# Optimization experiments

Hardware: AMD Instinct MI355X
Metric: run time of the kernel (lower is better)

The kernel has to match this reference:

```python
import jax, jax.numpy as jnp
import numpy as np

B, P, K = 32, 1024, 16  # clouds, points per cloud, neighbors


def setup_inputs() -> dict:
    key = jax.random.key(0)
    ks = jax.random.split(key, 5)
    N, C, H, D = B * P, 64, 128, 3
    x = jax.random.normal(ks[0], (N, C), dtype=jnp.float32)
    pos = jax.random.normal(ks[1], (N, D), dtype=jnp.float32)
    batch = jnp.arange(N, dtype=jnp.int64) // P  # cloud id per node
    W_e = jax.random.normal(ks[2], (2 * C, H), dtype=jnp.float32) * 0.05
    b_e = jnp.zeros((H,), dtype=jnp.float32)
    W_sc = jax.random.normal(ks[3], (C, H), dtype=jnp.float32) * 0.05
    b_sc = jnp.zeros((H,), dtype=jnp.float32)
    return {"x": x, "pos": pos, "batch": batch,
            "W_e": W_e, "b_e": b_e, "W_sc": W_sc, "b_sc": b_sc}


def _knn_idx(posb):
    # posb: [B, P, D] -> idx [B, P, K]: K nearest neighbors (sources) per target node,
    # within each cloud, excluding self (loop=False in torch_geometric.knn_graph).
    sq = jnp.sum(posb * posb, axis=-1)                       # [B, P]
    d2 = sq[:, :, None] + sq[:, None, :] - 2.0 * jnp.einsum('bid,bjd->bij', posb, posb)
    d2 = d2 + jnp.eye(P, dtype=posb.dtype)[None] * jnp.finfo(posb.dtype).max / 2
    _, idx = jax.lax.top_k(-d2, K)                           # [B, P, K]
    return idx


def reference(x, pos, batch, W_e, b_e, W_sc, b_sc):
    C = x.shape[-1]
    xb = x.reshape(B, P, C)
    posb = pos.reshape(B, P, -1)
    idx = _knn_idx(posb)                                     # [B, P, K]
    # gather neighbor (source) features per target node
    x_j = jax.vmap(lambda xc, ic: xc[ic])(xb, idx)           # [B, P, K, C]
    x_i = xb[:, :, None, :]                                  # [B, P, 1, C]
    # EdgeConv message: nn([x_i, x_j - x_i]), here Linear + ReLU
    e = jnp.concatenate([jnp.broadcast_to(x_i, x_j.shape), x_j - x_i], axis=-1)  # [B,P,K,2C]
    msg = jax.nn.relu(jnp.einsum('bpke,eh->bpkh', e, W_e) + b_e)
    agg = jnp.max(msg, axis=2)                               # max aggregation -> [B, P, H]
    shortcut = x @ W_sc + b_sc                               # [N, H]
    out = agg.reshape(-1, agg.shape[-1]) + shortcut
    return out
```

## Files before the change

### kernel.cpp

```cpp
#include <hip/hip_runtime.h>
#include <float.h>
#include <stdint.h>

#define BATCHES 32
#define P 1024
#define KNN 16
#define C 64
#define H 128
#define N (BATCHES * P)
#define NCOLS 384
#define SPLITS 8
#define CPS 128

typedef short short8 __attribute__((ext_vector_type(8)));
typedef float floatx4 __attribute__((ext_vector_type(4)));

__device__ __forceinline__ unsigned short f2bf(float f) {
    unsigned u = __float_as_uint(f);
    unsigned r = (u + 0x7FFF + ((u >> 16) & 1)) >> 16;
    return (unsigned short)r;
}

__global__ __launch_bounds__(256) void prep_w(
    const float* __restrict__ W_e, const float* __restrict__ b_e,
    const float* __restrict__ W_sc, const float* __restrict__ b_sc,
    unsigned short* __restrict__ WT, float* __restrict__ bias)
{
    int i = blockIdx.x * 256 + threadIdx.x;
    int col = i >> 6, c = i & 63;
    float w;
    if (col < 128)      w = W_e[c * 128 + col] - W_e[(64 + c) * 128 + col];
    else if (col < 256) w = W_e[(64 + c) * 128 + (col - 128)];
    else                w = W_sc[c * 128 + (col - 256)];
    WT[col * 64 + c] = f2bf(w);
    if (c == 0) {
        bias[col] = (col < 128) ? b_e[col] : (col < 256 ? 0.0f : b_sc[col - 256]);
    }
}

__global__ __launch_bounds__(512) void knn_kernel(
    const float* __restrict__ pos, int* __restrict__ idx_out)
{
    int t = threadIdx.x;
    int q = t & 63, s = t >> 6;
    int batch = blockIdx.x >> 4;
    int qblk  = blockIdx.x & 15;
    int iloc  = qblk * 64 + q;

    __shared__ float4 spos[P];
    __shared__ float  lists[SPLITS][16][64];
    __shared__ unsigned short elist[SPLITS][16][64];
    __shared__ int    ecnt[SPLITS][64];
    __shared__ float  Tq[64];

    const float* pb = pos + (size_t)batch * P * 3;
    for (int j = t; j < P; j += 512) {
        float x = pb[j * 3 + 0], y = pb[j * 3 + 1], z = pb[j * 3 + 2];
        float sq = __fadd_rn(__fadd_rn(__fmul_rn(x, x), __fmul_rn(y, y)),
                             __fmul_rn(z, z));
        spos[j] = make_float4(x, y, z, sq);
    }
    __syncthreads();

    float4 me = spos[iloc];
    float d[16];
#pragma unroll
    for (int k = 0; k < 16; ++k) d[k] = FLT_MAX;

    const int j0 = s * CPS;
    for (int jj = 0; jj < CPS; ++jj) {
        int j = j0 + jj;
        float4 c = spos[j];
        float dot = __fadd_rn(__fadd_rn(__fmul_rn(me.x, c.x), __fmul_rn(me.y, c.y)),
                              __fmul_rn(me.z, c.z));
        float d2 = __fadd_rn(__fadd_rn(me.w, c.w), __fmul_rn(-2.0f, dot));
        if (j == iloc) d2 = FLT_MAX;
#pragma unroll
        for (int k = 15; k >= 1; --k)
            d[k] = __builtin_amdgcn_fmed3f(d[k - 1], d2, d[k]);
        d[0] = fminf(d[0], d2);
    }
#pragma unroll
    for (int k = 0; k < 16; ++k) lists[s][k][q] = d[k];
    __syncthreads();

    if (s == 0) {
        float v0 = lists[0][0][q], v1 = lists[1][0][q];
        float v2 = lists[2][0][q], v3 = lists[3][0][q];
        float v4 = lists[4][0][q], v5 = lists[5][0][q];
        float v6 = lists[6][0][q], v7 = lists[7][0][q];
        int p0 = 0, p1 = 0, p2 = 0, p3 = 0, p4 = 0, p5 = 0, p6 = 0, p7 = 0;
        float T = 0.0f;
        for (int k = 0; k < 16; ++k) {
            float mn = fminf(fminf(fminf(v0, v1), fminf(v2, v3)),
                             fminf(fminf(v4, v5), fminf(v6, v7)));
            if      (v0 == mn) { p0++; v0 = (p0 < 16) ? lists[0][p0][q] : FLT_MAX; }
            else if (v1 == mn) { p1++; v1 = (p1 < 16) ? lists[1][p1][q] : FLT_MAX; }
            else if (v2 == mn) { p2++; v2 = (p2 < 16) ? lists[2][p2][q] : FLT_MAX; }
            else if (v3 == mn) { p3++; v3 = (p3 < 16) ? lists[3][p3][q] : FLT_MAX; }
            else if (v4 == mn) { p4++; v4 = (p4 < 16) ? lists[4][p4][q] : FLT_MAX; }
            else if (v5 == mn) { p5++; v5 = (p5 < 16) ? lists[5][p5][q] : FLT_MAX; }
            else if (v6 == mn) { p6++; v6 = (p6 < 16) ? lists[6][p6][q] : FLT_MAX; }
            else               { p7++; v7 = (p7 < 16) ? lists[7][p7][q] : FLT_MAX; }
            T = mn;
        }
        Tq[q] = T;
    }
    __syncthreads();
    float T = Tq[q];

    int cnt = 0;
    for (int jj = 0; jj < CPS; ++jj) {
        int j = j0 + jj;
        float4 c = spos[j];
        float dot = __fadd_rn(__fadd_rn(__fmul_rn(me.x, c.x), __fmul_rn(me.y, c.y)),
                              __fmul_rn(me.z, c.z));
        float d2 = __fadd_rn(__fadd_rn(me.w, c.w), __fmul_rn(-2.0f, dot));
        if (j == iloc) d2 = FLT_MAX;
        if (d2 <= T && cnt < 16) {
            elist[s][cnt][q] = (unsigned short)j;
            cnt++;
        }
    }
    ecnt[s][q] = cnt;
    __syncthreads();

    if (s == 0) {
        int out = 0;
        int gbase = (batch * P + iloc) * KNN;
        int base  = batch * P;
        for (int ss = 0; ss < SPLITS; ++ss) {
            int cc = ecnt[ss][q];
            for (int k = 0; k < cc && out < KNN; ++k) {
                idx_out[gbase + out] = base + (int)elist[ss][k][q];
                out++;
            }
        }
    }
}

__global__ __launch_bounds__(256) void gemm_kernel(
    const float* __restrict__ X, const unsigned short* __restrict__ WT,
    const float* __restrict__ bias,
    unsigned short* __restrict__ U, unsigned short* __restrict__ V,
    unsigned short* __restrict__ S)
{
    int t = threadIdx.x;
    int wave = t >> 6, l = t & 63;
    int m0 = (blockIdx.x * 4 + wave) * 16;
    int lm = l & 15, kg = l >> 4;

    const float4* arow = (const float4*)(X + (size_t)(m0 + lm) * 64 + kg * 8);
    float4 f0 = arow[0], f1 = arow[1];
    float4 f2 = arow[8], f3 = arow[9];
    short8 a0, a1;
    a0[0] = (short)f2bf(f0.x); a0[1] = (short)f2bf(f0.y);
    a0[2] = (short)f2bf(f0.z); a0[3] = (short)f2bf(f0.w);
    a0[4] = (short)f2bf(f1.x); a0[5] = (short)f2bf(f1.y);
    a0[6] = (short)f2bf(f1.z); a0[7] = (short)f2bf(f1.w);
    a1[0] = (short)f2bf(f2.x); a1[1] = (short)f2bf(f2.y);
    a1[2] = (short)f2bf(f2.z); a1[3] = (short)f2bf(f2.w);
    a1[4] = (short)f2bf(f3.x); a1[5] = (short)f2bf(f3.y);
    a1[6] = (short)f2bf(f3.z); a1[7] = (short)f2bf(f3.w);

#pragma unroll 4
    for (int nt = 0; nt < 24; ++nt) {
        const short8* brow = (const short8*)(WT + (size_t)(nt * 16 + lm) * 64 + kg * 8);
        short8 b0 = brow[0];
        short8 b1 = brow[4];
        floatx4 acc = {0.0f, 0.0f, 0.0f, 0.0f};
        acc = __builtin_amdgcn_mfma_f32_16x16x32_bf16(a0, b0, acc, 0, 0, 0);
        acc = __builtin_amdgcn_mfma_f32_16x16x32_bf16(a1, b1, acc, 0, 0, 0);

        int col = nt * 16 + lm;
        float bv = bias[col];
        unsigned short* dst; int cl;
        if (col < 128)      { dst = U; cl = col; }
        else if (col < 256) { dst = V; cl = col - 128; }
        else                { dst = S; cl = col - 256; }
#pragma unroll
        for (int r = 0; r < 4; ++r) {
            int row = m0 + kg * 4 + r;
            dst[(size_t)row * H + cl] = f2bf(acc[r] + bv);
        }
    }
}

__global__ __launch_bounds__(256) void final_kernel(
    const int* __restrict__ idx, const unsigned short* __restrict__ U,
    const unsigned short* __restrict__ V, const unsigned short* __restrict__ S,
    float* __restrict__ out)
{
    int t = threadIdx.x;
    int pin = t >> 6, c = t & 63;
    size_t p = (size_t)blockIdx.x * 4 + pin;

    __shared__ int nbr[4][KNN];
    if (t < 64) nbr[t >> 4][t & 15] = idx[(size_t)blockIdx.x * 4 * KNN + t];
    __syncthreads();

    unsigned uu = ((const unsigned*)(U + p * H))[c];
    unsigned ss = ((const unsigned*)(S + p * H))[c];
    float u0 = __uint_as_float(uu << 16);
    float u1 = __uint_as_float(uu & 0xFFFF0000u);
    float s0 = __uint_as_float(ss << 16);
    float s1 = __uint_as_float(ss & 0xFFFF0000u);

    float m0 = -FLT_MAX, m1 = -FLT_MAX;
#pragma unroll
    for (int k = 0; k < KNN; ++k) {
        unsigned vv = ((const unsigned*)(V + (size_t)nbr[pin][k] * H))[c];
        m0 = fmaxf(m0, __uint_as_float(vv << 16));
        m1 = fmaxf(m1, __uint_as_float(vv & 0xFFFF0000u));
    }

    float2 o;
    o.x = fmaxf(u0 + m0, 0.0f) + s0;
    o.y = fmaxf(u1 + m1, 0.0f) + s1;
    ((float2*)(out + p * H))[c] = o;
}

extern "C" void kernel_launch(void* const* d_in, const int* in_sizes, int n_in,
                              void* d_out, int out_size, void* d_ws, size_t ws_size,
                              hipStream_t stream)
{
    const float* x    = (const float*)d_in[0];
    const float* pos  = (const float*)d_in[1];
    const float* W_e  = (const float*)d_in[3];
    const float* b_e  = (const float*)d_in[4];
    const float* W_sc = (const float*)d_in[5];
    const float* b_sc = (const float*)d_in[6];
    float* out = (float*)d_out;

    char* ws = (char*)d_ws;
    const size_t OFF_IDX  = 0;
    const size_t OFF_U    = 2ull << 20;
    const size_t OFF_V    = OFF_U + (8ull << 20);
    const size_t OFF_S    = OFF_V + (8ull << 20);
    const size_t OFF_WT   = OFF_S + (8ull << 20);
    const size_t OFF_BIAS = OFF_WT + (64ull << 10);

    int*            idx  = (int*)(ws + OFF_IDX);
    unsigned short* U    = (unsigned short*)(ws + OFF_U);
    unsigned short* V    = (unsigned short*)(ws + OFF_V);
    unsigned short* S    = (unsigned short*)(ws + OFF_S);
    unsigned short* WT   = (unsigned short*)(ws + OFF_WT);
    float*          bias = (float*)(ws + OFF_BIAS);

    prep_w<<<(NCOLS * C) / 256, 256, 0, stream>>>(W_e, b_e, W_sc, b_sc, WT, bias);
    knn_kernel<<<BATCHES * 16, 512, 0, stream>>>(pos, idx);
    gemm_kernel<<<(N / 16) / 4, 256, 0, stream>>>(x, WT, bias, U, V, S);
    final_kernel<<<N / 4, 256, 0, stream>>>(idx, U, V, S, out);
}
```

Before: 152.0 us.

## Fuse kNN, GEMM and aggregation into one cooperative kernel with grid sync

Merges the kNN, the MFMA GEMM and the max-aggregation kernels into one cooperative kernel of 512 blocks. Each block keeps its U/S tiles and neighbor indices in aliased shared memory and writes only V to global memory, then calls a grid-wide sync before gathering neighbors. This removes two kernel launches and the global round trips for idx, U and S. The cost is a grid barrier, a cooperative launch that requires all 512 blocks to be co-resident, and shared-memory reuse that could limit occupancy.

```diff
diff --git a/kernel.cpp b/kernel.cpp
--- a/kernel.cpp
+++ b/kernel.cpp
@@ -1,6 +1,9 @@
 #include <hip/hip_runtime.h>
+#include <hip/hip_cooperative_groups.h>
 #include <float.h>
 #include <stdint.h>
+
+namespace cg = cooperative_groups;
 
 #define BATCHES 32
 #define P 1024
@@ -38,39 +41,57 @@
     }
 }
 
-__global__ __launch_bounds__(512) void knn_kernel(
-    const float* __restrict__ pos, int* __restrict__ idx_out)
+struct alignas(16) F4 { float x, y, z, w; };
+
+struct PA {
+    F4    spos[P];
+    float lists[SPLITS][16][64];
+    unsigned short elist[SPLITS][16][64];
+    int   ecnt[SPLITS][64];
+    float Tq[64];
+};
+struct PB {
+    unsigned short Ubuf[64][H];
+    unsigned short Sbuf[64][H];
+    unsigned short Vst [64][H];
+};
+
+__global__ __launch_bounds__(512, 4) void fused_kernel(
+    const float* __restrict__ pos, const float* __restrict__ X,
+    const unsigned short* __restrict__ WT, const float* __restrict__ bias,
+    unsigned short* __restrict__ V, float* __restrict__ out)
 {
+    __shared__ __align__(16) char smraw[sizeof(PA)];
+    PA* A  = (PA*)smraw;
+    PB* Bm = (PB*)smraw;
+    __shared__ int idxL[64][KNN];
+
     int t = threadIdx.x;
     int q = t & 63, s = t >> 6;
-    int batch = blockIdx.x >> 4;
-    int qblk  = blockIdx.x & 15;
+    int blk = blockIdx.x;
+    int batch = blk >> 4;
+    int qblk  = blk & 15;
     int iloc  = qblk * 64 + q;
-
-    __shared__ float4 spos[P];
-    __shared__ float  lists[SPLITS][16][64];
-    __shared__ unsigned short elist[SPLITS][16][64];
-    __shared__ int    ecnt[SPLITS][64];
-    __shared__ float  Tq[64];
 
     const float* pb = pos + (size_t)batch * P * 3;
     for (int j = t; j < P; j += 512) {
         float x = pb[j * 3 + 0], y = pb[j * 3 + 1], z = pb[j * 3 + 2];
         float sq = __fadd_rn(__fadd_rn(__fmul_rn(x, x), __fmul_rn(y, y)),
                              __fmul_rn(z, z));
-        spos[j] = make_float4(x, y, z, sq);
-    }
-    __syncthreads();
-
-    float4 me = spos[iloc];
+        A->spos[j] = F4{x, y, z, sq};
+    }
+    __syncthreads();
+
+    F4 me = A->spos[iloc];
     float d[16];
 #pragma unroll
     for (int k = 0; k < 16; ++k) d[k] = FLT_MAX;
 
     const int j0 = s * CPS;
+#pragma unroll 2
     for (int jj = 0; jj < CPS; ++jj) {
         int j = j0 + jj;
-        float4 c = spos[j];
+        F4 c = A->spos[j];
         float dot = __fadd_rn(__fadd_rn(__fmul_rn(me.x, c.x), __fmul_rn(me.y, c.y)),
                               __fmul_rn(me.z, c.z));
         float d2 = __fadd_rn(__fadd_rn(me.w, c.w), __fmul_rn(-2.0f, dot));
@@ -81,143 +102,143 @@
         d[0] = fminf(d[0], d2);
     }
 #pragma unroll
-    for (int k = 0; k < 16; ++k) lists[s][k][q] = d[k];
+    for (int k = 0; k < 16; ++k) A->lists[s][k][q] = d[k];
     __syncthreads();
 
     if (s == 0) {
-        float v0 = lists[0][0][q], v1 = lists[1][0][q];
-        float v2 = lists[2][0][q], v3 = lists[3][0][q];
-        float v4 = lists[4][0][q], v5 = lists[5][0][q];
-        float v6 = lists[6][0][q], v7 = lists[7][0][q];
+        float v0 = A->lists[0][0][q], v1 = A->lists[1][0][q];
+        float v2 = A->lists[2][0][q], v3 = A->lists[3][0][q];
+        float v4 = A->lists[4][0][q], v5 = A->lists[5][0][q];
+        float v6 = A->lists[6][0][q], v7 = A->lists[7][0][q];
         int p0 = 0, p1 = 0, p2 = 0, p3 = 0, p4 = 0, p5 = 0, p6 = 0, p7 = 0;
         float T = 0.0f;
         for (int k = 0; k < 16; ++k) {
             float mn = fminf(fminf(fminf(v0, v1), fminf(v2, v3)),
                              fminf(fminf(v4, v5), fminf(v6, v7)));
-            if      (v0 == mn) { p0++; v0 = (p0 < 16) ? lists[0][p0][q] : FLT_MAX; }
-            else if (v1 == mn) { p1++; v1 = (p1 < 16) ? lists[1][p1][q] : FLT_MAX; }
-            else if (v2 == mn) { p2++; v2 = (p2 < 16) ? lists[2][p2][q] : FLT_MAX; }
-            else if (v3 == mn) { p3++; v3 = (p3 < 16) ? lists[3][p3][q] : FLT_MAX; }
-            else if (v4 == mn) { p4++; v4 = (p4 < 16) ? lists[4][p4][q] : FLT_MAX; }
-            else if (v5 == mn) { p5++; v5 = (p5 < 16) ? lists[5][p5][q] : FLT_MAX; }
-            else if (v6 == mn) { p6++; v6 = (p6 < 16) ? lists[6][p6][q] : FLT_MAX; }
-            else               { p7++; v7 = (p7 < 16) ? lists[7][p7][q] : FLT_MAX; }
+            if      (v0 == mn) { p0++; v0 = (p0 < 16) ? A->lists[0][p0][q] : FLT_MAX; }
+            else if (v1 == mn) { p1++; v1 = (p1 < 16) ? A->lists[1][p1][q] : FLT_MAX; }
+            else if (v2 == mn) { p2++; v2 = (p2 < 16) ? A->lists[2][p2][q] : FLT_MAX; }
+            else if (v3 == mn) { p3++; v3 = (p3 < 16) ? A->lists[3][p3][q] : FLT_MAX; }
+            else if (v4 == mn) { p4++; v4 = (p4 < 16) ? A->lists[4][p4][q] : FLT_MAX; }
+            else if (v5 == mn) { p5++; v5 = (p5 < 16) ? A->lists[5][p5][q] : FLT_MAX; }
+            else if (v6 == mn) { p6++; v6 = (p6 < 16) ? A->lists[6][p6][q] : FLT_MAX; }
+            else               { p7++; v7 = (p7 < 16) ? A->lists[7][p7][q] : FLT_MAX; }
             T = mn;
         }
-        Tq[q] = T;
-    }
-    __syncthreads();
-    float T = Tq[q];
+        A->Tq[q] = T;
+    }
+    __syncthreads();
+    float T = A->Tq[q];
 
     int cnt = 0;
     for (int jj = 0; jj < CPS; ++jj) {
         int j = j0 + jj;
-        float4 c = spos[j];
+        F4 c = A->spos[j];
         float dot = __fadd_rn(__fadd_rn(__fmul_rn(me.x, c.x), __fmul_rn(me.y, c.y)),
                               __fmul_rn(me.z, c.z));
         float d2 = __fadd_rn(__fadd_rn(me.w, c.w), __fmul_rn(-2.0f, dot));
         if (j == iloc) d2 = FLT_MAX;
         if (d2 <= T && cnt < 16) {
-            elist[s][cnt][q] = (unsigned short)j;
+            A->elist[s][cnt][q] = (unsigned short)j;
             cnt++;
         }
     }
-    ecnt[s][q] = cnt;
+    A->ecnt[s][q] = cnt;
     __syncthreads();
 
     if (s == 0) {
-        int out = 0;
-        int gbase = (batch * P + iloc) * KNN;
-        int base  = batch * P;
+        int o = 0;
+        int base = batch * P;
+#pragma unroll
         for (int ss = 0; ss < SPLITS; ++ss) {
-            int cc = ecnt[ss][q];
-            for (int k = 0; k < cc && out < KNN; ++k) {
-                idx_out[gbase + out] = base + (int)elist[ss][k][q];
-                out++;
+            int cc = A->ecnt[ss][q];
+            for (int k = 0; k < cc && o < KNN; ++k) {
+                idxL[q][o] = base + (int)A->elist[ss][k][q];
+                o++;
             }
         }
     }
-}
-
-__global__ __launch_bounds__(256) void gemm_kernel(
-    const float* __restrict__ X, const unsigned short* __restrict__ WT,
-    const float* __restrict__ bias,
-    unsigned short* __restrict__ U, unsigned short* __restrict__ V,
-    unsigned short* __restrict__ S)
-{
-    int t = threadIdx.x;
-    int wave = t >> 6, l = t & 63;
-    int m0 = (blockIdx.x * 4 + wave) * 16;
-    int lm = l & 15, kg = l >> 4;
-
-    const float4* arow = (const float4*)(X + (size_t)(m0 + lm) * 64 + kg * 8);
-    float4 f0 = arow[0], f1 = arow[1];
-    float4 f2 = arow[8], f3 = arow[9];
-    short8 a0, a1;
-    a0[0] = (short)f2bf(f0.x); a0[1] = (short)f2bf(f0.y);
-    a0[2] = (short)f2bf(f0.z); a0[3] = (short)f2bf(f0.w);
-    a0[4] = (short)f2bf(f1.x); a0[5] = (short)f2bf(f1.y);
-    a0[6] = (short)f2bf(f1.z); a0[7] = (short)f2bf(f1.w);
-    a1[0] = (short)f2bf(f2.x); a1[1] = (short)f2bf(f2.y);
-    a1[2] = (short)f2bf(f2.z); a1[3] = (short)f2bf(f2.w);
-    a1[4] = (short)f2bf(f3.x); a1[5] = (short)f2bf(f3.y);
-    a1[6] = (short)f2bf(f3.z); a1[7] = (short)f2bf(f3.w);
+    __syncthreads();
+
+    {
+        int mt = s & 3, nh = s >> 2;
+        int m0 = blk * 64 + mt * 16;
+        int lm = q & 15, kg = q >> 4;
+
+        const float4* arow = (const float4*)(X + (size_t)(m0 + lm) * 64 + kg * 8);
+        float4 f0 = arow[0], f1 = arow[1];
+        float4 f2 = arow[8], f3 = arow[9];
+        short8 a0, a1;
+        a0[0] = (short)f2bf(f0.x); a0[1] = (short)f2bf(f0.y);
+        a0[2] = (short)f2bf(f0.z); a0[3] = (short)f2bf(f0.w);
+        a0[4] = (short)f2bf(f1.x); a0[5] = (short)f2bf(f1.y);
+        a0[6] = (short)f2bf(f1.z); a0[7] = (short)f2bf(f1.w);
+        a1[0] = (short)f2bf(f2.x); a1[1] = (short)f2bf(f2.y);
+        a1[2] = (short)f2bf(f2.z); a1[3] = (short)f2bf(f2.w);
+        a1[4] = (short)f2bf(f3.x); a1[5] = (short)f2bf(f3.y);
+        a1[6] = (short)f2bf(f3.z); a1[7] = (short)f2bf(f3.w);
 
 #pragma unroll 4
-    for (int nt = 0; nt < 24; ++nt) {
-        const short8* brow = (const short8*)(WT + (size_t)(nt * 16 + lm) * 64 + kg * 8);
-        short8 b0 = brow[0];
-        short8 b1 = brow[4];
-        floatx4 acc = {0.0f, 0.0f, 0.0f, 0.0f};
-        acc = __builtin_amdgcn_mfma_f32_16x16x32_bf16(a0, b0, acc, 0, 0, 0);
-        acc = __builtin_amdgcn_mfma_f32_16x16x32_bf16(a1, b1, acc, 0, 0, 0);
-
-        int col = nt * 16 + lm;
-        float bv = bias[col];
-        unsigned short* dst; int cl;
-        if (col < 128)      { dst = U; cl = col; }
-        else if (col < 256) { dst = V; cl = col - 128; }
-        else                { dst = S; cl = col - 256; }
-#pragma unroll
-        for (int r = 0; r < 4; ++r) {
-            int row = m0 + kg * 4 + r;
-            dst[(size_t)row * H + cl] = f2bf(acc[r] + bv);
-        }
-    }
-}
-
-__global__ __launch_bounds__(256) void final_kernel(
-    const int* __restrict__ idx, const unsigned short* __restrict__ U,
-    const unsigned short* __restrict__ V, const unsigned short* __restrict__ S,
-    float* __restrict__ out)
-{
-    int t = threadIdx.x;
-    int pin = t >> 6, c = t & 63;
-    size_t p = (size_t)blockIdx.x * 4 + pin;
-
-    __shared__ int nbr[4][KNN];
-    if (t < 64) nbr[t >> 4][t & 15] = idx[(size_t)blockIdx.x * 4 * KNN + t];
-    __syncthreads();
-
-    unsigned uu = ((const unsigned*)(U + p * H))[c];
-    unsigned ss = ((const unsigned*)(S + p * H))[c];
-    float u0 = __uint_as_float(uu << 16);
-    float u1 = __uint_as_float(uu & 0xFFFF0000u);
-    float s0 = __uint_as_float(ss << 16);
-    float s1 = __uint_as_float(ss & 0xFFFF0000u);
-
-    float m0 = -FLT_MAX, m1 = -FLT_MAX;
-#pragma unroll
-    for (int k = 0; k < KNN; ++k) {
-        unsigned vv = ((const unsigned*)(V + (size_t)nbr[pin][k] * H))[c];
-        m0 = fmaxf(m0, __uint_as_float(vv << 16));
-        m1 = fmaxf(m1, __uint_as_float(vv & 0xFFFF0000u));
-    }
-
-    float2 o;
-    o.x = fmaxf(u0 + m0, 0.0f) + s0;
-    o.y = fmaxf(u1 + m1, 0.0f) + s1;
-    ((float2*)(out + p * H))[c] = o;
+        for (int nt = nh * 12; nt < nh * 12 + 12; ++nt) {
+            const short8* brow = (const short8*)(WT + (size_t)(nt * 16 + lm) * 64 + kg * 8);
+            short8 b0 = brow[0];
+            short8 b1 = brow[4];
+            floatx4 acc = {0.0f, 0.0f, 0.0f, 0.0f};
+            acc = __builtin_amdgcn_mfma_f32_16x16x32_bf16(a0, b0, acc, 0, 0, 0);
+            acc = __builtin_amdgcn_mfma_f32_16x16x32_bf16(a1, b1, acc, 0, 0, 0);
+
+            int col = nt * 16 + lm;
+            float bv = bias[col];
+#pragma unroll
+            for (int r = 0; r < 4; ++r) {
+                int row = mt * 16 + kg * 4 + r;
+                unsigned short val = f2bf(acc[r] + bv);
+                if (col < 128)      Bm->Ubuf[row][col] = val;
+                else if (col < 256) Bm->Vst[row][col - 128] = val;
+                else                Bm->Sbuf[row][col - 256] = val;
+            }
+        }
+    }
+    __syncthreads();
+
+    {
+        const uint4* vs = (const uint4*)Bm->Vst;
+        uint4* vg = (uint4*)(V + (size_t)blk * 64 * H);
+        vg[t]       = vs[t];
+        vg[t + 512] = vs[t + 512];
+    }
+
+    cg::this_grid().sync();
+
+    {
+        int c2 = t & 63, pg = t >> 6;
+        const unsigned* Vu = (const unsigned*)V;
+#pragma unroll
+        for (int pp = 0; pp < 8; ++pp) {
+            int pl = pg * 8 + pp;
+            unsigned uu = ((const unsigned*)Bm->Ubuf)[pl * 64 + c2];
+            unsigned sv = ((const unsigned*)Bm->Sbuf)[pl * 64 + c2];
+            float u0 = __uint_as_float(uu << 16);
+            float u1 = __uint_as_float(uu & 0xFFFF0000u);
+            float s0 = __uint_as_float(sv << 16);
+            float s1 = __uint_as_float(sv & 0xFFFF0000u);
+
+            float m0 = -FLT_MAX, m1 = -FLT_MAX;
+#pragma unroll
+            for (int k = 0; k < KNN; ++k) {
+                int row = idxL[pl][k];
+                unsigned vv = Vu[(size_t)row * 64 + c2];
+                m0 = fmaxf(m0, __uint_as_float(vv << 16));
+                m1 = fmaxf(m1, __uint_as_float(vv & 0xFFFF0000u));
+            }
+
+            size_t p = (size_t)blk * 64 + pl;
+            float2 o;
+            o.x = fmaxf(u0 + m0, 0.0f) + s0;
+            o.y = fmaxf(u1 + m1, 0.0f) + s1;
+            ((float2*)out)[p * 64 + c2] = o;
+        }
+    }
 }
 
 extern "C" void kernel_launch(void* const* d_in, const int* in_sizes, int n_in,
@@ -233,22 +254,18 @@
     float* out = (float*)d_out;
 
     char* ws = (char*)d_ws;
-    const size_t OFF_IDX  = 0;
-    const size_t OFF_U    = 2ull << 20;
-    const size_t OFF_V    = OFF_U + (8ull << 20);
-    const size_t OFF_S    = OFF_V + (8ull << 20);
-    const size_t OFF_WT   = OFF_S + (8ull << 20);
-    const size_t OFF_BIAS = OFF_WT + (64ull << 10);
-
-    int*            idx  = (int*)(ws + OFF_IDX);
-    unsigned short* U    = (unsigned short*)(ws + OFF_U);
+    const size_t OFF_V    = 0;
+    const size_t OFF_WT   = 8ull << 20;
+    const size_t OFF_BIAS = OFF_WT + 49152;
+
     unsigned short* V    = (unsigned short*)(ws + OFF_V);
-    unsigned short* S    = (unsigned short*)(ws + OFF_S);
     unsigned short* WT   = (unsigned short*)(ws + OFF_WT);
     float*          bias = (float*)(ws + OFF_BIAS);
 
     prep_w<<<(NCOLS * C) / 256, 256, 0, stream>>>(W_e, b_e, W_sc, b_sc, WT, bias);
-    knn_kernel<<<BATCHES * 16, 512, 0, stream>>>(pos, idx);
-    gemm_kernel<<<(N / 16) / 4, 256, 0, stream>>>(x, WT, bias, U, V, S);
-    final_kernel<<<N / 4, 256, 0, stream>>>(idx, U, V, S, out);
-}
+
+    void* kargs[] = {(void*)&pos, (void*)&x, (void*)&WT, (void*)&bias,
+                     (void*)&V, (void*)&out};
+    hipLaunchCooperativeKernel((void*)fused_kernel, dim3(512), dim3(512),
+                               kargs, 0, stream);
+}
```

Result: slower. 217.4 us (+43.1%).
